# Kernel optimization log

Hardware: AMD Instinct MI355X
Metric: run time of the kernel (lower is better)

Reference implementation:

```python
import jax, jax.numpy as jnp
import numpy as np

B = 8192      # batch of matchups
L = 40        # history_len
HN = 32       # hist_numeric_dim
TE = 96       # team_embed_dim
SE = 32       # seed_embed_dim
HH = 64       # hist_hidden_dim
NH = 4        # num_heads
HD = HH // NH # head dim = 16
MID = 128     # middle_dim
BOX = 8       # box_score_dim
NT = 400      # num_teams
NS = 17       # num_seeds
TOWER_IN = TE + SE + 1 + 2 * HH  # 257
MERGED = 2 * MID                 # 256
EPS = 1e-5


def setup_inputs() -> dict:
    key = jax.random.key(0)
    ks = iter(jax.random.split(key, 80))
    nrm = lambda shape, s=0.05: (jax.random.normal(next(ks), shape, jnp.float32) * s)
    inp = {}
    inp['teamA_id'] = jax.random.randint(next(ks), (B,), 1, NT)
    inp['teamB_id'] = jax.random.randint(next(ks), (B,), 1, NT)
    inp['teamA_seed'] = jax.random.randint(next(ks), (B,), 0, NS)
    inp['teamB_seed'] = jax.random.randint(next(ks), (B,), 0, NS)
    inp['teamA_elo'] = 1500.0 + 200.0 * jax.random.normal(next(ks), (B,), jnp.float32)
    inp['teamB_elo'] = 1500.0 + 200.0 * jax.random.normal(next(ks), (B,), jnp.float32)
    inp['teamA_hist_numeric'] = jax.random.normal(next(ks), (B, L, HN), jnp.float32)
    inp['teamB_hist_numeric'] = jax.random.normal(next(ks), (B, L, HN), jnp.float32)
    inp['teamA_hist_opp_ids'] = jax.random.randint(next(ks), (B, L), 0, NT)
    inp['teamB_hist_opp_ids'] = jax.random.randint(next(ks), (B, L), 0, NT)
    # 0/1 padding mask; guarantee at least one valid game per row
    inp['teamA_hist_mask'] = (jax.random.uniform(next(ks), (B, L)) < 0.8).astype(jnp.float32).at[:, 0].set(1.0)
    inp['teamB_hist_mask'] = (jax.random.uniform(next(ks), (B, L)) < 0.8).astype(jnp.float32).at[:, 0].set(1.0)
    # parameters
    inp['team_emb'] = nrm((NT, TE), 0.1).at[0].set(0.0)  # padding_idx=0
    inp['seed_emb'] = nrm((NS, SE), 0.1)
    inp['conv_w'] = nrm((HH, HN + TE, 3))
    inp['conv_b'] = nrm((HH,))
    inp['cbn_g'] = jnp.ones((HH,)); inp['cbn_b'] = jnp.zeros((HH,))
    inp['cbn_rm'] = nrm((HH,), 0.01); inp['cbn_rv'] = jnp.ones((HH,))
    inp['hp_w'] = nrm((HH, HN + TE)); inp['hp_b'] = nrm((HH,))
    inp['qp_w'] = nrm((HH, TE)); inp['qp_b'] = nrm((HH,))
    inp['attn_in_w'] = nrm((3 * HH, HH)); inp['attn_in_b'] = nrm((3 * HH,))
    inp['attn_out_w'] = nrm((HH, HH)); inp['attn_out_b'] = nrm((HH,))
    inp['ln_g'] = jnp.ones((HH,)); inp['ln_b'] = jnp.zeros((HH,))
    inp['tw_w'] = nrm((MID, TOWER_IN)); inp['tw_b'] = nrm((MID,))
    inp['tbn_g'] = jnp.ones((MID,)); inp['tbn_b'] = jnp.zeros((MID,))
    inp['tbn_rm'] = nrm((MID,), 0.01); inp['tbn_rv'] = jnp.ones((MID,))
    inp['r1_w'] = nrm((MERGED, MERGED)); inp['r1_b'] = nrm((MERGED,))
    inp['r1bn_g'] = jnp.ones((MERGED,)); inp['r1bn_b'] = jnp.zeros((MERGED,))
    inp['r1bn_rm'] = nrm((MERGED,), 0.01); inp['r1bn_rv'] = jnp.ones((MERGED,))
    inp['r2_w'] = nrm((MERGED, MERGED)); inp['r2_b'] = nrm((MERGED,))
    inp['r2bn_g'] = jnp.ones((MERGED,)); inp['r2bn_b'] = jnp.zeros((MERGED,))
    inp['r2bn_rm'] = nrm((MERGED,), 0.01); inp['r2bn_rv'] = jnp.ones((MERGED,))
    inp['mu_w'] = nrm((BOX, MERGED)); inp['mu_b'] = nrm((BOX,))
    inp['lv_w'] = nrm((BOX, MERGED)); inp['lv_b'] = nrm((BOX,))
    inp['wl_w'] = nrm((1, MERGED)); inp['wl_b'] = nrm((1,))
    return inp


def _bn(x, g, b, rm, rv):
    # eval-mode BatchNorm over last axis
    return (x - rm) * jax.lax.rsqrt(rv + EPS) * g + b


def _ln(x, g, b):
    m = jnp.mean(x, axis=-1, keepdims=True)
    v = jnp.var(x, axis=-1, keepdims=True)
    return (x - m) * jax.lax.rsqrt(v + EPS) * g + b


def reference(teamA_id, teamB_id, teamA_seed, teamB_seed, teamA_elo, teamB_elo,
              teamA_hist_numeric, teamA_hist_opp_ids, teamA_hist_mask,
              teamB_hist_numeric, teamB_hist_opp_ids, teamB_hist_mask,
              team_emb, seed_emb, conv_w, conv_b, cbn_g, cbn_b, cbn_rm, cbn_rv,
              hp_w, hp_b, qp_w, qp_b, attn_in_w, attn_in_b, attn_out_w, attn_out_b,
              ln_g, ln_b, tw_w, tw_b, tbn_g, tbn_b, tbn_rm, tbn_rv,
              r1_w, r1_b, r1bn_g, r1bn_b, r1bn_rm, r1bn_rv,
              r2_w, r2_b, r2bn_g, r2bn_b, r2bn_rm, r2bn_rv,
              mu_w, mu_b, lv_w, lv_b, wl_w, wl_b):
    silu = jax.nn.silu

    def attend(q_emb, hn, opp, mask):
        m = mask[..., None]
        x = jnp.concatenate([hn * m, team_emb[opp] * m], axis=-1)      # [B,L,HN+TE]
        res = silu(x @ hp_w.T + hp_b)                                   # [B,L,HH]
        c = jax.lax.conv_general_dilated(
            x.transpose(0, 2, 1), conv_w, (1,), [(1, 1)],
            dimension_numbers=('NCH', 'OIH', 'NCH')) + conv_b[:, None]  # [B,HH,L]
        c = _bn(c.transpose(0, 2, 1), cbn_g, cbn_b, cbn_rm, cbn_rv)     # [B,L,HH]
        kv = silu(c + res)                                              # [B,L,HH]
        q = q_emb @ qp_w.T + qp_b                                       # [B,HH]
        wq, wk, wv = jnp.split(attn_in_w, 3, axis=0)
        bq, bk, bv = jnp.split(attn_in_b, 3, axis=0)
        qh = (q @ wq.T + bq).reshape(-1, NH, HD)
        kh = (kv @ wk.T + bk).reshape(-1, L, NH, HD)
        vh = (kv @ wv.T + bv).reshape(-1, L, NH, HD)
        scores = jnp.einsum('bhd,blhd->bhl', qh, kh) / np.float32(np.sqrt(HD))
        scores = jnp.where(mask[:, None, :] > 0.0, scores, -1e9)
        a = jax.nn.softmax(scores, axis=-1)
        o = jnp.einsum('bhl,blhd->bhd', a, vh).reshape(-1, HH)
        o = o @ attn_out_w.T + attn_out_b
        return _ln(o + q, ln_g, ln_b)

    ea = team_emb[teamA_id]
    eb = team_emb[teamB_id]
    sa = seed_emb[teamA_seed]
    sb = seed_emb[teamB_seed]
    za = (teamA_elo[:, None] - 1500.0) / 400.0
    zb = (teamB_elo[:, None] - 1500.0) / 400.0

    aa = attend(ea, teamA_hist_numeric, teamA_hist_opp_ids, teamA_hist_mask)
    ab = attend(ea, teamB_hist_numeric, teamB_hist_opp_ids, teamB_hist_mask)
    bb = attend(eb, teamB_hist_numeric, teamB_hist_opp_ids, teamB_hist_mask)
    ba = attend(eb, teamA_hist_numeric, teamA_hist_opp_ids, teamA_hist_mask)

    ta = jnp.concatenate([ea, sa, za, aa, ab], axis=-1)
    tb = jnp.concatenate([eb, sb, zb, bb, ba], axis=-1)

    tower = lambda t: silu(_bn(t @ tw_w.T + tw_b, tbn_g, tbn_b, tbn_rm, tbn_rv))
    ra = tower(ta)
    rb = tower(tb)

    x = jnp.concatenate([ra - rb, ra * rb], axis=-1)
    x = silu(_bn(x @ r1_w.T + r1_b, r1bn_g, r1bn_b, r1bn_rm, r1bn_rv)) + x
    x = silu(_bn(x @ r2_w.T + r2_b, r2bn_g, r2bn_b, r2bn_rm, r2bn_rv)) + x

    box_mu = x @ mu_w.T + mu_b
    box_log_var = x @ lv_w.T + lv_b
    win_logit = (x @ wl_w.T + wl_b)[:, 0]
    return ((box_mu, box_log_var), win_logit)
```

## Files before the change

kernel.cpp:

```cpp
#include <hip/hip_runtime.h>
#include <stdint.h>

#define EPS 1e-5f

typedef __attribute__((ext_vector_type(8))) short short8;
typedef __attribute__((ext_vector_type(4))) float floatx4;
typedef __attribute__((ext_vector_type(4))) unsigned uintx4;
typedef unsigned short u16;

__device__ __forceinline__ u16 f2bf(float f) {
  unsigned u = __builtin_bit_cast(unsigned, f);
  u += 0x7fffu + ((u >> 16) & 1u);
  return (u16)(u >> 16);
}
__device__ __forceinline__ float bf2f(u16 h) {
  return __builtin_bit_cast(float, (unsigned)h << 16);
}
__device__ __forceinline__ unsigned pack2bf(float a, float b) {
  return (unsigned)f2bf(a) | ((unsigned)f2bf(b) << 16);
}
__device__ __forceinline__ float silu_f(float x) { return x / (1.f + __expf(-x)); }
__device__ __forceinline__ float wave_sum(float x) {
  for (int off = 32; off > 0; off >>= 1) x += __shfl_xor(x, off);
  return x;
}

__global__ void prep_kernel(const float* __restrict__ hp_w, const float* __restrict__ conv_w,
                            const float* __restrict__ attn_in_w,
                            const float* __restrict__ attn_out_w,
                            const float* __restrict__ tw_w, const float* __restrict__ r1_w,
                            const float* __restrict__ r2_w,
                            u16* __restrict__ w1f, u16* __restrict__ w2f,
                            float* __restrict__ woT,
                            float* __restrict__ twT, float* __restrict__ r1T,
                            float* __restrict__ r2T) {
  int t = blockIdx.x * 256 + threadIdx.x;
  if (t < 32768) {
    int j = t & 7, lane = (t >> 3) & 63, ks = (t >> 9) & 3, nt = t >> 11;
    int k = ks * 32 + ((lane >> 4) << 3) + j;
    int n = nt * 16 + (lane & 15);
    float v = (n < 64) ? hp_w[n * 128 + k]
                       : conv_w[((n - 64) & 63) * 384 + k * 3 + ((n - 64) >> 6)];
    w1f[t] = f2bf(v);
  }
  if (t < 8192) {
    int j = t & 7, lane = (t >> 3) & 63, ks = (t >> 9) & 1, nt = t >> 10;
    int k = ks * 32 + ((lane >> 4) << 3) + j;
    int n = nt * 16 + (lane & 15);
    w2f[t] = f2bf(attn_in_w[(64 + n) * 64 + k]);
  }
  if (t < 1024) {
    int j = t & 63, k4 = t >> 6;
#pragma unroll
    for (int i = 0; i < 4; ++i)
      woT[(k4 * 64 + j) * 4 + i] = attn_out_w[j * 64 + k4 * 4 + i];
  }
  if (t < 8320) {
    int mid = t & 127, k4 = t >> 7;
#pragma unroll
    for (int i = 0; i < 4; ++i) {
      int k = k4 * 4 + i;
      twT[t * 4 + i] = (k < 257) ? tw_w[mid * 257 + k] : 0.f;
    }
  }
  if (t < 16384) {
    int o = t & 255, k4 = t >> 8;
#pragma unroll
    for (int i = 0; i < 4; ++i) {
      r1T[t * 4 + i] = r1_w[o * 256 + k4 * 4 + i];
      r2T[t * 4 + i] = r2_w[o * 256 + k4 * 4 + i];
    }
  }
}

__global__ __launch_bounds__(64) void team_kernel(
    const float* __restrict__ temb, const float* __restrict__ qp_w,
    const float* __restrict__ qp_b, const float* __restrict__ attn_in_w,
    const float* __restrict__ attn_in_b,
    float* __restrict__ Qg, float* __restrict__ QHg) {
  __shared__ float e[96];
  __shared__ float qv[64];
  const int t = blockIdx.x;
  const int o = threadIdx.x;
  for (int i = o; i < 96; i += 64) e[i] = temb[t * 96 + i];
  __syncthreads();
  float acc = qp_b[o];
  for (int k = 0; k < 96; ++k) acc += e[k] * qp_w[o * 96 + k];
  qv[o] = acc;
  Qg[t * 64 + o] = acc;
  __syncthreads();
  float acc2 = attn_in_b[o];
  for (int k = 0; k < 64; ++k) acc2 += qv[k] * attn_in_w[o * 64 + k];
  QHg[t * 64 + o] = acc2;
}

__global__ __launch_bounds__(256, 2) void attn_kernel(
    const int* __restrict__ idA, const int* __restrict__ idB,
    const float* __restrict__ hnA, const float* __restrict__ hnB,
    const int* __restrict__ oppA, const int* __restrict__ oppB,
    const float* __restrict__ mskA, const float* __restrict__ mskB,
    const float* __restrict__ temb, const float* __restrict__ conv_b,
    const float* __restrict__ cbn_g, const float* __restrict__ cbn_b,
    const float* __restrict__ cbn_rm, const float* __restrict__ cbn_rv,
    const float* __restrict__ hp_b,
    const float* __restrict__ attn_in_b, const float* __restrict__ attn_out_b,
    const float* __restrict__ ln_g, const float* __restrict__ ln_b,
    const u16* __restrict__ w1f, const u16* __restrict__ w2f,
    const float* __restrict__ woT,
    const float* __restrict__ Qg, const float* __restrict__ QHg,
    float* __restrict__ ATT) {
  __shared__ __align__(16) u16 xb[48 * 136];
  __shared__ __align__(16) u16 ybuf[48 * 264];
  __shared__ __align__(16) u16 kvb[48 * 72];
  __shared__ float a_s[8][40];
  __shared__ __align__(16) float o_s[2][64];
  __shared__ float qh_s[2][64];
  float* KVP = (float*)ybuf;

  const int tid = threadIdx.x;
  const int lane = tid & 63;
  const int wv = tid >> 6;
  const int qd = lane >> 4;
  const int l16 = lane & 15;

  const int c2 = (tid & 31) * 2;
  const int lb = tid >> 5;
  const float pw_sc0 = rsqrtf(cbn_rv[c2] + EPS) * cbn_g[c2];
  const float pw_sc1 = rsqrtf(cbn_rv[c2 + 1] + EPS) * cbn_g[c2 + 1];
  const float pw_sh0 = cbn_b[c2] - cbn_rm[c2] * pw_sc0;
  const float pw_sh1 = cbn_b[c2 + 1] - cbn_rm[c2 + 1] * pw_sc1;
  const float pw_hpb0 = hp_b[c2], pw_hpb1 = hp_b[c2 + 1];
  const float pw_cvb0 = conv_b[c2], pw_cvb1 = conv_b[c2 + 1];
  const float lng = ln_g[lane], lnb = ln_b[lane];
  const float aob = attn_out_b[lane];

  for (int idx = tid; idx < 8 * 64; idx += 256)
    kvb[(40 + (idx >> 6)) * 72 + (idx & 63)] = 0;
  __syncthreads();

  short8 w1r[4][4];
#pragma unroll
  for (int ntl = 0; ntl < 4; ++ntl)
#pragma unroll
    for (int ks = 0; ks < 4; ++ks)
      w1r[ntl][ks] = *reinterpret_cast<const short8*>(
          w1f + (((wv * 4 + ntl) * 4 + ks) * 64 + lane) * 8);
  short8 w2r[2][2];
#pragma unroll
  for (int ntl = 0; ntl < 2; ++ntl)
#pragma unroll
    for (int ks = 0; ks < 2; ++ks)
      w2r[ntl][ks] = *reinterpret_cast<const short8*>(
          w2f + (((wv * 2 + ntl) * 2 + ks) * 64 + lane) * 8);

  unsigned xr[12];
  float mkr[3];
  {
    int np = blockIdx.x;
    int pb = np >> 1;
    const float* phn = (np & 1) ? hnB : hnA;
    const int* popp = (np & 1) ? oppB : oppA;
    const float* pmsk = (np & 1) ? mskB : mskA;
#pragma unroll
    for (int j = 0; j < 3; ++j) {
      int sidx = j * 256 + tid;
      int srow = sidx >> 4, scg = sidx & 15;
      if (srow < 40) {
        int mrow = pb * 40 + srow;
        mkr[j] = pmsk[mrow];
        const float* p = (scg < 4)
                             ? phn + (size_t)mrow * 32 + scg * 8
                             : temb + (size_t)popp[mrow] * 96 + (scg * 8 - 32);
        floatx4 f0 = *reinterpret_cast<const floatx4*>(p);
        floatx4 f1 = *reinterpret_cast<const floatx4*>(p + 4);
        xr[j * 4 + 0] = pack2bf(f0[0], f0[1]);
        xr[j * 4 + 1] = pack2bf(f0[2], f0[3]);
        xr[j * 4 + 2] = pack2bf(f1[0], f1[1]);
        xr[j * 4 + 3] = pack2bf(f1[2], f1[3]);
      } else {
        mkr[j] = 0.f;
        xr[j * 4 + 0] = xr[j * 4 + 1] = xr[j * 4 + 2] = xr[j * 4 + 3] = 0u;
      }
    }
  }

#pragma unroll 1
  for (int it = 0; it < 8; ++it) {
    int pair = blockIdx.x + it * 2048;
    int b = pair >> 1, s = pair & 1;

#pragma unroll
    for (int j = 0; j < 3; ++j) {
      int sidx = j * 256 + tid;
      bool keep = mkr[j] != 0.f;
      uintx4 v;
      v[0] = keep ? xr[j * 4 + 0] : 0u;
      v[1] = keep ? xr[j * 4 + 1] : 0u;
      v[2] = keep ? xr[j * 4 + 2] : 0u;
      v[3] = keep ? xr[j * 4 + 3] : 0u;
      *reinterpret_cast<uintx4*>(xb + (sidx >> 4) * 136 + (sidx & 15) * 8) = v;
    }
    float qreg = 0.f, qhreg = 0.f, m_l = 0.f;
    if (wv < 2) {
      int id = wv ? idB[b] : idA[b];
      qreg = Qg[id * 64 + lane];
      qhreg = QHg[id * 64 + lane];
      if (lane < 40) m_l = (s ? mskB : mskA)[b * 40 + lane];
    }
    __syncthreads();

#pragma unroll 1
    for (int mt = 0; mt < 3; ++mt) {
      short8 af[4];
#pragma unroll
      for (int ks = 0; ks < 4; ++ks)
        af[ks] = *reinterpret_cast<const short8*>(
            xb + (mt * 16 + l16) * 136 + ks * 32 + (qd << 3));
      floatx4 acc[4] = {};
#pragma unroll
      for (int ks = 0; ks < 4; ++ks)
#pragma unroll
        for (int ntl = 0; ntl < 4; ++ntl)
          acc[ntl] = __builtin_amdgcn_mfma_f32_16x16x32_bf16(
              af[ks], w1r[ntl][ks], acc[ntl], 0, 0, 0);
#pragma unroll
      for (int ntl = 0; ntl < 4; ++ntl)
#pragma unroll
        for (int r = 0; r < 4; ++r)
          ybuf[(mt * 16 + qd * 4 + r) * 264 + (wv * 4 + ntl) * 16 + l16] =
              f2bf(acc[ntl][r]);
    }
    __syncthreads();

    float pf[3][8];
    float mknew[3];
    {
      int np = (it < 7) ? pair + 2048 : pair;
      int pb = np >> 1;
      const float* phn = (np & 1) ? hnB : hnA;
      const int* popp = (np & 1) ? oppB : oppA;
      const float* pmsk = (np & 1) ? mskB : mskA;
#pragma unroll
      for (int j = 0; j < 3; ++j) {
        int sidx = j * 256 + tid;
        int srow = sidx >> 4, scg = sidx & 15;
        if (srow < 40) {
          int mrow = pb * 40 + srow;
          mknew[j] = pmsk[mrow];
          const float* p = (scg < 4)
                               ? phn + (size_t)mrow * 32 + scg * 8
                               : temb + (size_t)popp[mrow] * 96 + (scg * 8 - 32);
          *reinterpret_cast<floatx4*>(&pf[j][0]) = *reinterpret_cast<const floatx4*>(p);
          *reinterpret_cast<floatx4*>(&pf[j][4]) = *reinterpret_cast<const floatx4*>(p + 4);
        } else {
          mknew[j] = 0.f;
#pragma unroll
          for (int q = 0; q < 8; ++q) pf[j][q] = 0.f;
        }
      }
    }

#pragma unroll
    for (int t = 0; t < 5; ++t) {
      int l = lb + 8 * t;
      unsigned yhp = *reinterpret_cast<const unsigned*>(ybuf + l * 264 + c2);
      unsigned t0 = (l >= 1) ? *reinterpret_cast<const unsigned*>(ybuf + (l - 1) * 264 + 64 + c2) : 0u;
      unsigned t1 = *reinterpret_cast<const unsigned*>(ybuf + l * 264 + 128 + c2);
      unsigned t2 = *reinterpret_cast<const unsigned*>(ybuf + (l + 1) * 264 + 192 + c2);
      float res0 = silu_f(bf2f((u16)yhp) + pw_hpb0);
      float res1 = silu_f(bf2f((u16)(yhp >> 16)) + pw_hpb1);
      float c0 = bf2f((u16)t0) + bf2f((u16)t1) + bf2f((u16)t2) + pw_cvb0;
      float c1 = bf2f((u16)(t0 >> 16)) + bf2f((u16)(t1 >> 16)) + bf2f((u16)(t2 >> 16)) + pw_cvb1;
      float kv0 = silu_f(c0 * pw_sc0 + pw_sh0 + res0);
      float kv1 = silu_f(c1 * pw_sc1 + pw_sh1 + res1);
      *reinterpret_cast<unsigned*>(kvb + l * 72 + c2) = pack2bf(kv0, kv1);
    }
    __syncthreads();

    {
      const float kb0 = attn_in_b[64 + (wv * 2 + 0) * 16 + l16];
      const float kb1 = attn_in_b[64 + (wv * 2 + 1) * 16 + l16];
      floatx4 acc[3][2] = {};
#pragma unroll
      for (int mt = 0; mt < 3; ++mt) {
        short8 af[2];
#pragma unroll
        for (int ks = 0; ks < 2; ++ks)
          af[ks] = *reinterpret_cast<const short8*>(
              kvb + (mt * 16 + l16) * 72 + ks * 32 + (qd << 3));
#pragma unroll
        for (int ntl = 0; ntl < 2; ++ntl)
#pragma unroll
          for (int ks = 0; ks < 2; ++ks)
            acc[mt][ntl] = __builtin_amdgcn_mfma_f32_16x16x32_bf16(
                af[ks], w2r[ntl][ks], acc[mt][ntl], 0, 0, 0);
      }
#pragma unroll
      for (int mt = 0; mt < 3; ++mt)
#pragma unroll
        for (int ntl = 0; ntl < 2; ++ntl)
#pragma unroll
          for (int r = 0; r < 4; ++r) {
            int row = mt * 16 + qd * 4 + r;
            int col = (wv * 2 + ntl) * 16 + l16;
            KVP[row * 129 + col] = acc[mt][ntl][r] + (ntl ? kb1 : kb0);
          }
    }
    __syncthreads();

#pragma unroll
    for (int j = 0; j < 3; ++j) {
      xr[j * 4 + 0] = pack2bf(pf[j][0], pf[j][1]);
      xr[j * 4 + 1] = pack2bf(pf[j][2], pf[j][3]);
      xr[j * 4 + 2] = pack2bf(pf[j][4], pf[j][5]);
      xr[j * 4 + 3] = pack2bf(pf[j][6], pf[j][7]);
      mkr[j] = mknew[j];
    }

    if (wv < 2) {
      int qi = wv;
      qh_s[qi][lane] = qhreg;
      float a[4];
#pragma unroll
      for (int h = 0; h < 4; ++h) {
        float e = 0.f;
        if (lane < 40 && m_l > 0.f) {
          float s0 = 0.f, s1 = 0.f;
#pragma unroll
          for (int d = 0; d < 16; d += 2) {
            s0 += qh_s[qi][h * 16 + d] * KVP[lane * 129 + h * 16 + d];
            s1 += qh_s[qi][h * 16 + d + 1] * KVP[lane * 129 + h * 16 + d + 1];
          }
          e = __expf((s0 + s1) * 0.25f);
        }
        float sm = wave_sum(e);
        a[h] = e / sm;
      }
#pragma unroll
      for (int h = 0; h < 4; ++h)
        if (lane < 40) a_s[qi * 4 + h][lane] = a[h];
      {
        int p = qi * 4 + (lane >> 4);
        float v0 = 0.f, v1 = 0.f;
#pragma unroll
        for (int l = 0; l < 40; l += 2) {
          v0 += a_s[p][l] * KVP[l * 129 + 64 + lane];
          v1 += a_s[p][l + 1] * KVP[(l + 1) * 129 + 64 + lane];
        }
        o_s[qi][lane] = v0 + v1;
      }
      float acc0 = aob + qreg, acc1 = 0.f;
      const floatx4* wo4 = reinterpret_cast<const floatx4*>(woT);
#pragma unroll 8
      for (int k4 = 0; k4 < 16; ++k4) {
        floatx4 w4 = wo4[k4 * 64 + lane];
        floatx4 x4 = *reinterpret_cast<const floatx4*>(&o_s[qi][k4 * 4]);
        acc0 += x4[0] * w4[0] + x4[2] * w4[2];
        acc1 += x4[1] * w4[1] + x4[3] * w4[3];
      }
      float r = acc0 + acc1;
      float mean = wave_sum(r) * (1.f / 64.f);
      float dv = r - mean;
      float var = wave_sum(dv * dv) * (1.f / 64.f);
      float outv = dv * rsqrtf(var + EPS) * lng + lnb;
      ATT[((qi * 2 + s) * 8192 + b) * 64 + lane] = outv;
    }
  }
}

__global__ __launch_bounds__(256) void head_kernel(
    const int* __restrict__ idA, const int* __restrict__ idB,
    const int* __restrict__ seedA, const int* __restrict__ seedB,
    const float* __restrict__ eloA, const float* __restrict__ eloB,
    const float* __restrict__ temb, const float* __restrict__ semb,
    const float* __restrict__ twT, const float* __restrict__ tw_b,
    const float* __restrict__ tbn_g, const float* __restrict__ tbn_b,
    const float* __restrict__ tbn_rm, const float* __restrict__ tbn_rv,
    const float* __restrict__ r1T, const float* __restrict__ r1_b,
    const float* __restrict__ r1bn_g, const float* __restrict__ r1bn_b,
    const float* __restrict__ r1bn_rm, const float* __restrict__ r1bn_rv,
    const float* __restrict__ r2T, const float* __restrict__ r2_b,
    const float* __restrict__ r2bn_g, const float* __restrict__ r2bn_b,
    const float* __restrict__ r2bn_rm, const float* __restrict__ r2bn_rv,
    const float* __restrict__ mu_w, const float* __restrict__ mu_b,
    const float* __restrict__ lv_w, const float* __restrict__ lv_b,
    const float* __restrict__ wl_w, const float* __restrict__ wl_b,
    const float* __restrict__ ATT, float* __restrict__ out) {
  __shared__ __align__(16) float tv[2][8][260];
  __shared__ __align__(16) float rr[2][8][128];
  __shared__ __align__(16) float xv[8][256];
  __shared__ __align__(16) float xw[8][256];
  const int tid = threadIdx.x;
  const int b0 = blockIdx.x * 8;

  for (int idx = tid; idx < 2 * 8 * 260; idx += 256) {
    int k = idx % 260;
    int bi = (idx / 260) & 7;
    int team = idx / (260 * 8);
    int b = b0 + bi;
    float v;
    if (k < 96) v = temb[(team ? idB[b] : idA[b]) * 96 + k];
    else if (k < 128) v = semb[(team ? seedB[b] : seedA[b]) * 32 + (k - 96)];
    else if (k == 128) v = ((team ? eloB[b] : eloA[b]) - 1500.f) * (1.f / 400.f);
    else if (k < 193) v = ATT[((team * 2 + team) * 8192 + b) * 64 + (k - 129)];
    else if (k < 257) v = ATT[((team * 2 + (1 - team)) * 8192 + b) * 64 + (k - 193)];
    else v = 0.f;
    tv[team][bi][k] = v;
  }
  __syncthreads();

  {
    int team = tid >> 7, mid = tid & 127;
    const floatx4* twv = reinterpret_cast<const floatx4*>(twT);
    float acc[8];
#pragma unroll
    for (int bi = 0; bi < 8; ++bi) acc[bi] = tw_b[mid];
#pragma unroll 2
    for (int k4 = 0; k4 < 65; ++k4) {
      floatx4 w4 = twv[k4 * 128 + mid];
      floatx4 x4[8];
#pragma unroll
      for (int bi = 0; bi < 8; ++bi)
        x4[bi] = *reinterpret_cast<const floatx4*>(&tv[team][bi][k4 * 4]);
#pragma unroll
      for (int bi = 0; bi < 8; ++bi)
        acc[bi] += x4[bi][0] * w4[0] + x4[bi][1] * w4[1] +
                   x4[bi][2] * w4[2] + x4[bi][3] * w4[3];
    }
    float sc = rsqrtf(tbn_rv[mid] + EPS) * tbn_g[mid];
    float sh = tbn_b[mid] - tbn_rm[mid] * sc;
#pragma unroll
    for (int bi = 0; bi < 8; ++bi) rr[team][bi][mid] = silu_f(acc[bi] * sc + sh);
  }
  __syncthreads();
  {
    int o = tid;
#pragma unroll
    for (int bi = 0; bi < 8; ++bi)
      xv[bi][o] = (o < 128) ? (rr[0][bi][o] - rr[1][bi][o])
                            : (rr[0][bi][o - 128] * rr[1][bi][o - 128]);
  }
  __syncthreads();
  {
    int o = tid;
    const floatx4* r1v = reinterpret_cast<const floatx4*>(r1T);
    float acc[8];
#pragma unroll
    for (int bi = 0; bi < 8; ++bi) acc[bi] = r1_b[o];
#pragma unroll 2
    for (int k4 = 0; k4 < 64; ++k4) {
      floatx4 w4 = r1v[k4 * 256 + o];
      floatx4 x4[8];
#pragma unroll
      for (int bi = 0; bi < 8; ++bi)
        x4[bi] = *reinterpret_cast<const floatx4*>(&xv[bi][k4 * 4]);
#pragma unroll
      for (int bi = 0; bi < 8; ++bi)
        acc[bi] += x4[bi][0] * w4[0] + x4[bi][1] * w4[1] +
                   x4[bi][2] * w4[2] + x4[bi][3] * w4[3];
    }
    float sc = rsqrtf(r1bn_rv[o] + EPS) * r1bn_g[o];
    float sh = r1bn_b[o] - r1bn_rm[o] * sc;
#pragma unroll
    for (int bi = 0; bi < 8; ++bi) xw[bi][o] = silu_f(acc[bi] * sc + sh) + xv[bi][o];
  }
  __syncthreads();
  {
    int o = tid;
    const floatx4* r2v = reinterpret_cast<const floatx4*>(r2T);
    float acc[8];
#pragma unroll
    for (int bi = 0; bi < 8; ++bi) acc[bi] = r2_b[o];
#pragma unroll 2
    for (int k4 = 0; k4 < 64; ++k4) {
      floatx4 w4 = r2v[k4 * 256 + o];
      floatx4 x4[8];
#pragma unroll
      for (int bi = 0; bi < 8; ++bi)
        x4[bi] = *reinterpret_cast<const floatx4*>(&xw[bi][k4 * 4]);
#pragma unroll
      for (int bi = 0; bi < 8; ++bi)
        acc[bi] += x4[bi][0] * w4[0] + x4[bi][1] * w4[1] +
                   x4[bi][2] * w4[2] + x4[bi][3] * w4[3];
    }
    float sc = rsqrtf(r2bn_rv[o] + EPS) * r2bn_g[o];
    float sh = r2bn_b[o] - r2bn_rm[o] * sc;
#pragma unroll
    for (int bi = 0; bi < 8; ++bi) xv[bi][o] = silu_f(acc[bi] * sc + sh) + xw[bi][o];
  }
  __syncthreads();
  if (tid < 136) {
    int bi = tid / 17, j = tid % 17;
    const float* wrow = (j < 8) ? (mu_w + j * 256) : (j < 16) ? (lv_w + (j - 8) * 256) : wl_w;
    const floatx4* wrow4 = reinterpret_cast<const floatx4*>(wrow);
    float acc = (j < 8) ? mu_b[j] : (j < 16) ? lv_b[j - 8] : wl_b[0];
    for (int k4 = 0; k4 < 64; ++k4) {
      floatx4 x4 = *reinterpret_cast<const floatx4*>(&xv[bi][k4 * 4]);
      floatx4 w4 = wrow4[k4];
      acc += x4[0] * w4[0] + x4[1] * w4[1] + x4[2] * w4[2] + x4[3] * w4[3];
    }
    int b = b0 + bi;
    if (j < 8) out[b * 8 + j] = acc;
    else if (j < 16) out[65536 + b * 8 + (j - 8)] = acc;
    else out[131072 + b] = acc;
  }
}

extern "C" void kernel_launch(void* const* d_in, const int* in_sizes, int n_in,
                              void* d_out, int out_size, void* d_ws, size_t ws_size,
                              hipStream_t stream) {
  const int* idA = (const int*)d_in[0];
  const int* idB = (const int*)d_in[1];
  const int* seedA = (const int*)d_in[2];
  const int* seedB = (const int*)d_in[3];
  const float* eloA = (const float*)d_in[4];
  const float* eloB = (const float*)d_in[5];
  const float* hnA = (const float*)d_in[6];
  const float* hnB = (const float*)d_in[7];
  const int* oppA = (const int*)d_in[8];
  const int* oppB = (const int*)d_in[9];
  const float* mskA = (const float*)d_in[10];
  const float* mskB = (const float*)d_in[11];
  const float* temb = (const float*)d_in[12];
  const float* semb = (const float*)d_in[13];
  const float* conv_w = (const float*)d_in[14];
  const float* conv_b = (const float*)d_in[15];
  const float* cbn_g = (const float*)d_in[16];
  const float* cbn_b = (const float*)d_in[17];
  const float* cbn_rm = (const float*)d_in[18];
  const float* cbn_rv = (const float*)d_in[19];
  const float* hp_w = (const float*)d_in[20];
  const float* hp_b = (const float*)d_in[21];
  const float* qp_w = (const float*)d_in[22];
  const float* qp_b = (const float*)d_in[23];
  const float* attn_in_w = (const float*)d_in[24];
  const float* attn_in_b = (const float*)d_in[25];
  const float* attn_out_w = (const float*)d_in[26];
  const float* attn_out_b = (const float*)d_in[27];
  const float* ln_g = (const float*)d_in[28];
  const float* ln_b = (const float*)d_in[29];
  const float* tw_w = (const float*)d_in[30];
  const float* tw_b = (const float*)d_in[31];
  const float* tbn_g = (const float*)d_in[32];
  const float* tbn_b = (const float*)d_in[33];
  const float* tbn_rm = (const float*)d_in[34];
  const float* tbn_rv = (const float*)d_in[35];
  const float* r1_w = (const float*)d_in[36];
  const float* r1_b = (const float*)d_in[37];
  const float* r1bn_g = (const float*)d_in[38];
  const float* r1bn_b = (const float*)d_in[39];
  const float* r1bn_rm = (const float*)d_in[40];
  const float* r1bn_rv = (const float*)d_in[41];
  const float* r2_w = (const float*)d_in[42];
  const float* r2_b = (const float*)d_in[43];
  const float* r2bn_g = (const float*)d_in[44];
  const float* r2bn_b = (const float*)d_in[45];
  const float* r2bn_rm = (const float*)d_in[46];
  const float* r2bn_rv = (const float*)d_in[47];
  const float* mu_w = (const float*)d_in[48];
  const float* mu_b = (const float*)d_in[49];
  const float* lv_w = (const float*)d_in[50];
  const float* lv_b = (const float*)d_in[51];
  const float* wl_w = (const float*)d_in[52];
  const float* wl_b = (const float*)d_in[53];

  char* ws = (char*)d_ws;
  u16* w1f = (u16*)(ws + 0);
  u16* w2f = (u16*)(ws + 65536);
  float* woT = (float*)(ws + 81920);
  float* Qg = (float*)(ws + 98304);
  float* QHg = (float*)(ws + 200704);
  float* twT = (float*)(ws + 303104);
  float* r1T = (float*)(ws + 436224);
  float* r2T = (float*)(ws + 698368);
  float* ATT = (float*)(ws + 960512);

  prep_kernel<<<256, 256, 0, stream>>>(hp_w, conv_w, attn_in_w, attn_out_w,
                                       tw_w, r1_w, r2_w,
                                       w1f, w2f, woT, twT, r1T, r2T);
  team_kernel<<<400, 64, 0, stream>>>(temb, qp_w, qp_b, attn_in_w, attn_in_b, Qg, QHg);
  attn_kernel<<<2048, 256, 0, stream>>>(idA, idB, hnA, hnB, oppA, oppB, mskA, mskB,
                                        temb, conv_b, cbn_g, cbn_b, cbn_rm, cbn_rv,
                                        hp_b, attn_in_b, attn_out_b, ln_g, ln_b,
                                        w1f, w2f, woT, Qg, QHg, ATT);
  head_kernel<<<1024, 256, 0, stream>>>(idA, idB, seedA, seedB, eloA, eloB, temb, semb,
                                        twT, tw_b, tbn_g, tbn_b, tbn_rm, tbn_rv,
                                        r1T, r1_b, r1bn_g, r1bn_b, r1bn_rm, r1bn_rv,
                                        r2T, r2_b, r2bn_g, r2bn_b, r2bn_rm, r2bn_rv,
                                        mu_w, mu_b, lv_w, lv_b, wl_w, wl_b,
                                        ATT, (float*)d_out);
}
```

Before: 581.9 us.

## Fuse conv taps into MFMA accumulation via shifted row reads, drop ybuf staging

Reorders the first weight matrix by conv tap so each wave computes one channel group, and forms the 3-tap conv by issuing MFMAs on row-shifted A fragments from a zero-padded input buffer. Conv plus BN plus residual SiLU are then applied straight from accumulators, which removes the bf16 ybuf round trip through shared memory and one barrier. Per-iteration Q/QH/mask loads are moved to the end of the previous iteration as a prefetch, and the bias loads are hoisted out of the loop. The trade-off is more A-fragment LDS reads per MFMA, and a separate fp32 KVP buffer that raises shared-memory use and may reduce occupancy.

```diff
diff --git a/kernel.cpp b/kernel.cpp
--- a/kernel.cpp
+++ b/kernel.cpp
@@ -36,11 +36,10 @@
                             float* __restrict__ r2T) {
   int t = blockIdx.x * 256 + threadIdx.x;
   if (t < 32768) {
-    int j = t & 7, lane = (t >> 3) & 63, ks = (t >> 9) & 3, nt = t >> 11;
+    int j = t & 7, lane = (t >> 3) & 63, ks = (t >> 9) & 3, nt = (t >> 11) & 3, tp = t >> 13;
     int k = ks * 32 + ((lane >> 4) << 3) + j;
-    int n = nt * 16 + (lane & 15);
-    float v = (n < 64) ? hp_w[n * 128 + k]
-                       : conv_w[((n - 64) & 63) * 384 + k * 3 + ((n - 64) >> 6)];
+    int c = nt * 16 + (lane & 15);
+    float v = (tp == 3) ? hp_w[c * 128 + k] : conv_w[c * 384 + k * 3 + tp];
     w1f[t] = f2bf(v);
   }
   if (t < 8192) {
@@ -109,13 +108,12 @@
     const float* __restrict__ woT,
     const float* __restrict__ Qg, const float* __restrict__ QHg,
     float* __restrict__ ATT) {
-  __shared__ __align__(16) u16 xb[48 * 136];
-  __shared__ __align__(16) u16 ybuf[48 * 264];
+  __shared__ __align__(16) u16 xs[50 * 136];
   __shared__ __align__(16) u16 kvb[48 * 72];
+  __shared__ __align__(16) float KVP[40 * 129];
   __shared__ float a_s[8][40];
   __shared__ __align__(16) float o_s[2][64];
   __shared__ float qh_s[2][64];
-  float* KVP = (float*)ybuf;
 
   const int tid = threadIdx.x;
   const int lane = tid & 63;
@@ -123,28 +121,29 @@
   const int qd = lane >> 4;
   const int l16 = lane & 15;
 
-  const int c2 = (tid & 31) * 2;
-  const int lb = tid >> 5;
-  const float pw_sc0 = rsqrtf(cbn_rv[c2] + EPS) * cbn_g[c2];
-  const float pw_sc1 = rsqrtf(cbn_rv[c2 + 1] + EPS) * cbn_g[c2 + 1];
-  const float pw_sh0 = cbn_b[c2] - cbn_rm[c2] * pw_sc0;
-  const float pw_sh1 = cbn_b[c2 + 1] - cbn_rm[c2 + 1] * pw_sc1;
-  const float pw_hpb0 = hp_b[c2], pw_hpb1 = hp_b[c2 + 1];
-  const float pw_cvb0 = conv_b[c2], pw_cvb1 = conv_b[c2 + 1];
+  const int c_lane = wv * 16 + l16;
+  const float sc_c = rsqrtf(cbn_rv[c_lane] + EPS) * cbn_g[c_lane];
+  const float sh_c = cbn_b[c_lane] - cbn_rm[c_lane] * sc_c;
+  const float hpb_c = hp_b[c_lane];
+  const float cvb_c = conv_b[c_lane];
   const float lng = ln_g[lane], lnb = ln_b[lane];
   const float aob = attn_out_b[lane];
-
-  for (int idx = tid; idx < 8 * 64; idx += 256)
-    kvb[(40 + (idx >> 6)) * 72 + (idx & 63)] = 0;
+  const float kb0 = attn_in_b[64 + (wv * 2 + 0) * 16 + l16];
+  const float kb1 = attn_in_b[64 + (wv * 2 + 1) * 16 + l16];
+
+  if (tid < 136) {
+    xs[tid] = 0;
+    xs[49 * 136 + tid] = 0;
+  }
   __syncthreads();
 
   short8 w1r[4][4];
 #pragma unroll
-  for (int ntl = 0; ntl < 4; ++ntl)
+  for (int tp = 0; tp < 4; ++tp)
 #pragma unroll
     for (int ks = 0; ks < 4; ++ks)
-      w1r[ntl][ks] = *reinterpret_cast<const short8*>(
-          w1f + (((wv * 4 + ntl) * 4 + ks) * 64 + lane) * 8);
+      w1r[tp][ks] = *reinterpret_cast<const short8*>(
+          w1f + (((tp * 4 + wv) * 4 + ks) * 64 + lane) * 8);
   short8 w2r[2][2];
 #pragma unroll
   for (int ntl = 0; ntl < 2; ++ntl)
@@ -184,6 +183,15 @@
     }
   }
 
+  float qreg = 0.f, qhreg = 0.f, m_l = 0.f;
+  if (wv < 2) {
+    int b0i = blockIdx.x >> 1, s0 = blockIdx.x & 1;
+    int id0 = wv ? idB[b0i] : idA[b0i];
+    qreg = Qg[id0 * 64 + lane];
+    qhreg = QHg[id0 * 64 + lane];
+    if (lane < 40) m_l = (s0 ? mskB : mskA)[b0i * 40 + lane];
+  }
+
 #pragma unroll 1
   for (int it = 0; it < 8; ++it) {
     int pair = blockIdx.x + it * 2048;
@@ -198,37 +206,7 @@
       v[1] = keep ? xr[j * 4 + 1] : 0u;
       v[2] = keep ? xr[j * 4 + 2] : 0u;
       v[3] = keep ? xr[j * 4 + 3] : 0u;
-      *reinterpret_cast<uintx4*>(xb + (sidx >> 4) * 136 + (sidx & 15) * 8) = v;
-    }
-    float qreg = 0.f, qhreg = 0.f, m_l = 0.f;
-    if (wv < 2) {
-      int id = wv ? idB[b] : idA[b];
-      qreg = Qg[id * 64 + lane];
-      qhreg = QHg[id * 64 + lane];
-      if (lane < 40) m_l = (s ? mskB : mskA)[b * 40 + lane];
-    }
-    __syncthreads();
-
-#pragma unroll 1
-    for (int mt = 0; mt < 3; ++mt) {
-      short8 af[4];
-#pragma unroll
-      for (int ks = 0; ks < 4; ++ks)
-        af[ks] = *reinterpret_cast<const short8*>(
-            xb + (mt * 16 + l16) * 136 + ks * 32 + (qd << 3));
-      floatx4 acc[4] = {};
-#pragma unroll
-      for (int ks = 0; ks < 4; ++ks)
-#pragma unroll
-        for (int ntl = 0; ntl < 4; ++ntl)
-          acc[ntl] = __builtin_amdgcn_mfma_f32_16x16x32_bf16(
-              af[ks], w1r[ntl][ks], acc[ntl], 0, 0, 0);
-#pragma unroll
-      for (int ntl = 0; ntl < 4; ++ntl)
-#pragma unroll
-        for (int r = 0; r < 4; ++r)
-          ybuf[(mt * 16 + qd * 4 + r) * 264 + (wv * 4 + ntl) * 16 + l16] =
-              f2bf(acc[ntl][r]);
+      *reinterpret_cast<uintx4*>(xs + ((sidx >> 4) + 1) * 136 + (sidx & 15) * 8) = v;
     }
     __syncthreads();
 
@@ -260,26 +238,30 @@
       }
     }
 
-#pragma unroll
-    for (int t = 0; t < 5; ++t) {
-      int l = lb + 8 * t;
-      unsigned yhp = *reinterpret_cast<const unsigned*>(ybuf + l * 264 + c2);
-      unsigned t0 = (l >= 1) ? *reinterpret_cast<const unsigned*>(ybuf + (l - 1) * 264 + 64 + c2) : 0u;
-      unsigned t1 = *reinterpret_cast<const unsigned*>(ybuf + l * 264 + 128 + c2);
-      unsigned t2 = *reinterpret_cast<const unsigned*>(ybuf + (l + 1) * 264 + 192 + c2);
-      float res0 = silu_f(bf2f((u16)yhp) + pw_hpb0);
-      float res1 = silu_f(bf2f((u16)(yhp >> 16)) + pw_hpb1);
-      float c0 = bf2f((u16)t0) + bf2f((u16)t1) + bf2f((u16)t2) + pw_cvb0;
-      float c1 = bf2f((u16)(t0 >> 16)) + bf2f((u16)(t1 >> 16)) + bf2f((u16)(t2 >> 16)) + pw_cvb1;
-      float kv0 = silu_f(c0 * pw_sc0 + pw_sh0 + res0);
-      float kv1 = silu_f(c1 * pw_sc1 + pw_sh1 + res1);
-      *reinterpret_cast<unsigned*>(kvb + l * 72 + c2) = pack2bf(kv0, kv1);
+#pragma unroll 1
+    for (int mt = 0; mt < 3; ++mt) {
+      floatx4 ach = {0.f, 0.f, 0.f, 0.f};
+      floatx4 acv = {0.f, 0.f, 0.f, 0.f};
+#pragma unroll
+      for (int ks = 0; ks < 4; ++ks) {
+        const u16* base = xs + (mt * 16 + l16) * 136 + ks * 32 + (qd << 3);
+        short8 af0 = *reinterpret_cast<const short8*>(base);
+        short8 af1 = *reinterpret_cast<const short8*>(base + 136);
+        short8 af2 = *reinterpret_cast<const short8*>(base + 272);
+        acv = __builtin_amdgcn_mfma_f32_16x16x32_bf16(af0, w1r[0][ks], acv, 0, 0, 0);
+        acv = __builtin_amdgcn_mfma_f32_16x16x32_bf16(af1, w1r[1][ks], acv, 0, 0, 0);
+        acv = __builtin_amdgcn_mfma_f32_16x16x32_bf16(af2, w1r[2][ks], acv, 0, 0, 0);
+        ach = __builtin_amdgcn_mfma_f32_16x16x32_bf16(af1, w1r[3][ks], ach, 0, 0, 0);
+      }
+#pragma unroll
+      for (int r = 0; r < 4; ++r) {
+        float kv = silu_f(silu_f(ach[r] + hpb_c) + (acv[r] + cvb_c) * sc_c + sh_c);
+        kvb[(mt * 16 + qd * 4 + r) * 72 + c_lane] = f2bf(kv);
+      }
     }
     __syncthreads();
 
     {
-      const float kb0 = attn_in_b[64 + (wv * 2 + 0) * 16 + l16];
-      const float kb1 = attn_in_b[64 + (wv * 2 + 1) * 16 + l16];
       floatx4 acc[3][2] = {};
 #pragma unroll
       for (int mt = 0; mt < 3; ++mt) {
@@ -302,8 +284,9 @@
 #pragma unroll
           for (int r = 0; r < 4; ++r) {
             int row = mt * 16 + qd * 4 + r;
-            int col = (wv * 2 + ntl) * 16 + l16;
-            KVP[row * 129 + col] = acc[mt][ntl][r] + (ntl ? kb1 : kb0);
+            if (row < 40)
+              KVP[row * 129 + (wv * 2 + ntl) * 16 + l16] =
+                  acc[mt][ntl][r] + (ntl ? kb1 : kb0);
           }
     }
     __syncthreads();
@@ -364,6 +347,14 @@
       float var = wave_sum(dv * dv) * (1.f / 64.f);
       float outv = dv * rsqrtf(var + EPS) * lng + lnb;
       ATT[((qi * 2 + s) * 8192 + b) * 64 + lane] = outv;
+
+      if (it < 7) {
+        int bn = b + 1024;
+        int idn = wv ? idB[bn] : idA[bn];
+        qreg = Qg[idn * 64 + lane];
+        qhreg = QHg[idn * 64 + lane];
+        m_l = (lane < 40) ? (s ? mskB : mskA)[bn * 40 + lane] : 0.f;
+      }
     }
   }
 }
```

New measurement: 550.6 us. 1.06x faster.
